# Performance work log

Hardware: AMD Instinct MI355X
Metric: run time of the kernel (lower is better)

Reference implementation:

```python
import jax, jax.numpy as jnp
import numpy as np

V, E, H0, H1 = 32000, 512, 1024, 1024
B, S = 32, 128


def setup_inputs() -> dict:
    key = jax.random.key(0)
    ks = jax.random.split(key, 10)
    s = 0.02
    tokens = jax.random.randint(ks[0], (B, S), 0, V)
    emb = jax.random.normal(ks[1], (V, E), dtype=jnp.float32) * s
    W0 = jax.random.normal(ks[2], (E, H0), dtype=jnp.float32) * s
    U0 = jax.random.normal(ks[3], (H0, H0), dtype=jnp.float32) * s
    b0 = jnp.zeros((H0,), dtype=jnp.float32)
    W1 = jax.random.normal(ks[4], (H0, H1), dtype=jnp.float32) * s
    U1 = jax.random.normal(ks[5], (H1, H1), dtype=jnp.float32) * s
    b1 = jnp.zeros((H1,), dtype=jnp.float32)
    Wd = jax.random.normal(ks[6], (H1, V), dtype=jnp.float32) * s
    bd = jnp.zeros((V,), dtype=jnp.float32)
    return {"tokens": tokens, "emb": emb, "W0": W0, "U0": U0, "b0": b0,
            "W1": W1, "U1": U1, "b1": b1, "Wd": Wd, "bd": bd}


def reference(tokens, emb, W0, U0, b0, W1, U1, b1, Wd, bd):
    # Embedding lookup: [B, S, E]
    x = emb[tokens]
    # Stacked SimpleRNN: h_t = tanh(x W + h U + b), layer1 feeds layer2 per step.
    xt = jnp.swapaxes(x, 0, 1)  # [S, B, E] for scan over time

    def step(carry, x_t):
        h0, h1 = carry
        h0 = jnp.tanh(x_t @ W0 + h0 @ U0 + b0)
        h1 = jnp.tanh(h0 @ W1 + h1 @ U1 + b1)
        return (h0, h1), h1

    batch = tokens.shape[0]
    init = (jnp.zeros((batch, W0.shape[1]), dtype=x.dtype),
            jnp.zeros((batch, W1.shape[1]), dtype=x.dtype))
    _, ys = jax.lax.scan(step, init, xt)  # ys: [S, B, H1]
    ys = jnp.swapaxes(ys, 0, 1)  # [B, S, H1]
    # Final dense to vocab logits: [B, S, V]
    return ys @ Wd + bd
```

## Files before the change

### kernel.cpp

```cpp
#include <hip/hip_runtime.h>
#include <hip/hip_bf16.h>
#include <cstdint>

typedef __attribute__((ext_vector_type(8))) short bf16x8;
typedef __attribute__((ext_vector_type(4))) float f32x4;
typedef __attribute__((ext_vector_type(4))) unsigned int u32x4;

#define V_ 32000
#define E_ 512
#define H_ 1024
#define B_ 32
#define S_ 128

#define L1WG 16
#define L2WG 32
#define NWGS 48

typedef __attribute__((address_space(1))) unsigned int* gas1_t;
typedef __attribute__((address_space(3))) unsigned int* las3_t;
__device__ __forceinline__ void load_lds16(const void* g, void* l) {
  __builtin_amdgcn_global_load_lds((gas1_t)g, (las3_t)l, 16, 0, 0);
}

__device__ __forceinline__ void ldx4_sc(u32x4* d, const void* p) {
  asm volatile("global_load_dwordx4 %0, %1, off sc0 sc1" : "=v"(*d) : "v"(p) : "memory");
}
__device__ __forceinline__ unsigned ld_sc(const unsigned* p) {
  unsigned d;
  asm volatile("global_load_dword %0, %1, off sc0 sc1\n\ts_waitcnt vmcnt(0)"
               : "=v"(d) : "v"(p) : "memory");
  return d;
}
__device__ __forceinline__ void st_swap(unsigned* p, unsigned v) {
  asm volatile("global_atomic_swap %0, %1, off sc1" :: "v"(p), "v"(v) : "memory");
}
__device__ __forceinline__ void st_swap2(uint2* p, uint2 v) {
  asm volatile("global_atomic_swap_x2 %0, %1, off sc1" :: "v"(p), "v"(v) : "memory");
}
#define WAITVM0()                                     \
  asm volatile("s_waitcnt vmcnt(0)" ::: "memory");    \
  __builtin_amdgcn_sched_barrier(0)

__device__ __forceinline__ unsigned short bfbits(float x) {
  __hip_bfloat16 b = __float2bfloat16(x);
  union { __hip_bfloat16 b; unsigned short u; } c;
  c.b = b;
  return c.u;
}

__device__ __forceinline__ uint2 pack_rows(const float f[4], int lane, int j) {
  uint2 v2[4];
#pragma unroll
  for (int r = 0; r < 4; ++r) {
    const float o = __shfl_xor(f[r], 1);
    const float lo = (lane & 1) ? o : f[r];
    const float hi = (lane & 1) ? f[r] : o;
    const unsigned pk = (unsigned)bfbits(lo) | ((unsigned)bfbits(hi) << 16);
    const unsigned q2 = __shfl_xor(pk, 2);
    v2[r].x = (j & 2) ? q2 : pk;
    v2[r].y = (j & 2) ? pk : q2;
  }
  const int rs = lane & 3;
  return rs == 0 ? v2[0] : rs == 1 ? v2[1] : rs == 2 ? v2[2] : v2[3];
}

__global__ __launch_bounds__(256) void transpose_f32_bf16(
    const float* __restrict__ src, __hip_bfloat16* __restrict__ dst, int R, int C) {
  __shared__ float tile[32][33];
  const int c0 = blockIdx.x << 5, r0 = blockIdx.y << 5;
  const int tx = threadIdx.x & 31, ty = threadIdx.x >> 5;
#pragma unroll
  for (int i = 0; i < 32; i += 8)
    tile[ty + i][tx] = src[(size_t)(r0 + ty + i) * C + (c0 + tx)];
  __syncthreads();
#pragma unroll
  for (int i = 0; i < 32; i += 8)
    dst[(size_t)(c0 + ty + i) * R + (r0 + tx)] = __float2bfloat16(tile[tx][ty + i]);
}

__global__ __launch_bounds__(256) void gather_embed(
    const int* __restrict__ tokens, const float* __restrict__ emb,
    __hip_bfloat16* __restrict__ Xg) {
  const int r = blockIdx.x;
  const int t = r >> 5, b = r & 31;
  const int tok = tokens[b * S_ + t];
  const float* e = emb + (size_t)tok * E_;
  __hip_bfloat16* o = Xg + (size_t)r * E_;
  for (int k = threadIdx.x; k < E_; k += 256) o[k] = __float2bfloat16(e[k]);
}

__global__ __launch_bounds__(256) void make_frag_w(
    const float* __restrict__ W, __hip_bfloat16* __restrict__ F) {
  const int idx = blockIdx.x * 256 + threadIdx.x;
  const int lane = idx & 63, kb = (idx >> 6) & 31, g = idx >> 11;
  const int j = (g << 4) + (lane & 15);
  const int kbase = (kb << 5) + ((lane >> 4) << 3);
  __hip_bfloat16* o = F + (size_t)idx * 8;
#pragma unroll
  for (int e = 0; e < 8; ++e) o[e] = __float2bfloat16(W[(size_t)(kbase + e) * H_ + j]);
}

__global__ __launch_bounds__(256) void gemm_bf16_tn(
    const __hip_bfloat16* __restrict__ A, const __hip_bfloat16* __restrict__ Bt,
    const float* __restrict__ bias, float* __restrict__ C, int M, int N, int K) {
  __shared__ __hip_bfloat16 ldsA[128 * 64];
  __shared__ __hip_bfloat16 ldsB[128 * 64];
  const int nwg = gridDim.x * gridDim.y;
  int L = blockIdx.y * gridDim.x + blockIdx.x;
  L = ((L & 7) * (nwg >> 3)) + (L >> 3);
  const int m0 = (L / gridDim.x) << 7;
  const int n0 = (L % gridDim.x) << 7;
  const int tid = threadIdx.x, wave = tid >> 6, lane = tid & 63;
  const int wr = wave >> 1, wc = wave & 1;
  f32x4 acc[4][4];
#pragma unroll
  for (int i = 0; i < 4; ++i)
#pragma unroll
    for (int jj = 0; jj < 4; ++jj) acc[i][jj] = (f32x4){0.f, 0.f, 0.f, 0.f};

  for (int k0 = 0; k0 < K; k0 += 64) {
#pragma unroll
    for (int i = 0; i < 4; ++i) {
      const int c = i * 4 + wave;
      const int idx = (c << 6) + lane;
      const int row = idx >> 3, kk = (idx & 7) << 3;
      load_lds16(A + (size_t)(m0 + row) * K + (k0 + kk), ldsA + c * 512);
      load_lds16(Bt + (size_t)(n0 + row) * K + (k0 + kk), ldsB + c * 512);
    }
    __syncthreads();
#pragma unroll
    for (int ks = 0; ks < 2; ++ks) {
      bf16x8 af[4], bfr[4];
#pragma unroll
      for (int mi = 0; mi < 4; ++mi)
        af[mi] = *(const bf16x8*)(ldsA + (((wr << 6) + (mi << 4) + (lane & 15)) << 6) +
                                  (ks << 5) + ((lane >> 4) << 3));
#pragma unroll
      for (int ni = 0; ni < 4; ++ni)
        bfr[ni] = *(const bf16x8*)(ldsB + (((wc << 6) + (ni << 4) + (lane & 15)) << 6) +
                                   (ks << 5) + ((lane >> 4) << 3));
#pragma unroll
      for (int mi = 0; mi < 4; ++mi)
#pragma unroll
        for (int ni = 0; ni < 4; ++ni)
          acc[mi][ni] =
              __builtin_amdgcn_mfma_f32_16x16x32_bf16(af[mi], bfr[ni], acc[mi][ni], 0, 0, 0);
    }
    __syncthreads();
  }
#pragma unroll
  for (int mi = 0; mi < 4; ++mi) {
#pragma unroll
    for (int ni = 0; ni < 4; ++ni) {
      const int n = n0 + (wc << 6) + (ni << 4) + (lane & 15);
      const float bn = bias[n];
#pragma unroll
      for (int r = 0; r < 4; ++r) {
        const int m = m0 + (wr << 6) + (mi << 4) + ((lane >> 4) << 2) + r;
        C[(size_t)m * N + n] = acc[mi][ni][r] + bn;
      }
    }
  }
}

__global__ __launch_bounds__(512, 2) void rnn_recur(
    const __hip_bfloat16* __restrict__ U0f, const __hip_bfloat16* __restrict__ W1f,
    const __hip_bfloat16* __restrict__ U1f, const float* __restrict__ xw,
    const float* __restrict__ b1,
    __hip_bfloat16* __restrict__ h0buf,
    __hip_bfloat16* __restrict__ h1buf,
    __hip_bfloat16* __restrict__ Y,
    unsigned* __restrict__ flags) {
  __shared__ char smem[135168];
  char* sA0 = smem;
  char* sA1 = smem + 65536;
  float* pad = (float*)(smem + 131072);

  const int g = blockIdx.x;
  const bool isL1 = (g < L1WG);
  const int tid = threadIdx.x, wave = tid >> 6, lane = tid & 63;
  const int mi = wave & 1;
  const int cg = isL1 ? (wave >> 1) : ((wave >> 1) & 1);
  const int mat = isL1 ? 0 : (wave >> 2);
  const int colbase = isL1 ? (g << 6) : ((g - L1WG) << 5);
  const int j = colbase + (cg << 4) + (lane & 15);
  const int gg = (colbase >> 4) + cg;
  const int rowbase = (mi << 4) + ((lane >> 4) << 2);
  const int rs = lane & 3;
  const int ra = (mi << 4) + (lane & 15);
  const int q4 = (lane >> 4) << 4;
  const float b1j = b1[j];

  const __hip_bfloat16* wb = isL1 ? U0f : (mat == 0 ? W1f : U1f);
  bf16x8 wfr[32];
#pragma unroll
  for (int kb = 0; kb < 32; ++kb)
    wfr[kb] = *(const bf16x8*)(wb + (size_t)((((gg << 5) + kb) << 6) + lane) * 8);

  if (!isL1) {
    for (int i = tid; i < 4096; i += 512) *(uint4*)(sA1 + i * 16) = (uint4){0u, 0u, 0u, 0u};
  }
  __syncthreads();

  const int stg_row = tid >> 7;
  const int stg_colb = (tid & 127) << 4;
  const unsigned* fpoll = flags + ((lane < NWGS ? lane : NWGS - 1) << 4);

  if (isL1) {
    for (int p = 0; p < S_; ++p) {
      const float* xrow = xw + ((size_t)p << 15);
      float xv[4];
#pragma unroll
      for (int r = 0; r < 4; ++r) xv[r] = xrow[(rowbase + r) * H_ + j];
      if (p >= 1) {
        const unsigned tgt =
            (lane < L1WG) ? (unsigned)p : (p >= 3 ? (unsigned)(p - 3) : 0u);
        unsigned v;
        do { v = ld_sc(fpoll); } while (__any(v < tgt));
        const char* src0 = (const char*)(h0buf + ((size_t)((p - 1) & 3) << 15));
        u32x4 t0[8];
#pragma unroll
        for (int i = 0; i < 8; ++i) ldx4_sc(&t0[i], src0 + (size_t)(((i << 9) + tid) << 4));
        WAITVM0();
#pragma unroll
        for (int i = 0; i < 8; ++i) {
          const int row = stg_row + (i << 2);
          *(u32x4*)(sA0 + (row << 11) + (stg_colb ^ ((row & 7) << 4))) = t0[i];
        }
        __syncthreads();
      }
      f32x4 acc = {0.f, 0.f, 0.f, 0.f};
      if (p >= 1) {
#pragma unroll
        for (int kb = 0; kb < 32; ++kb) {
          bf16x8 a = *(const bf16x8*)(
              sA0 + (ra << 11) + ((((kb << 6) + q4)) ^ ((ra & 7) << 4)));
          acc = __builtin_amdgcn_mfma_f32_16x16x32_bf16(a, wfr[kb], acc, 0, 0, 0);
        }
      }
      float f[4];
#pragma unroll
      for (int r = 0; r < 4; ++r) f[r] = tanhf(acc[r] + xv[r]);
      uint2 vsel = pack_rows(f, lane, j);
      uint2* h4 = (uint2*)(h0buf + ((size_t)(p & 3) << 15));
      st_swap2(h4 + (rowbase + rs) * (H_ / 4) + (j >> 2), vsel);
      WAITVM0();
      __syncthreads();
      if (tid == 0) st_swap(flags + (g << 4), (unsigned)(p + 1));
    }
  } else {
    for (int t = 0; t < S_; ++t) {
      {
        const unsigned tgt = (lane < L1WG) ? (unsigned)(t + 1) : (unsigned)t;
        unsigned v;
        do { v = ld_sc(fpoll); } while (__any(v < tgt));
      }
      {
        const char* src0 = (const char*)(h0buf + ((size_t)(t & 3) << 15));
        u32x4 t0[8], t1[8];
#pragma unroll
        for (int i = 0; i < 8; ++i) ldx4_sc(&t0[i], src0 + (size_t)(((i << 9) + tid) << 4));
        if (t >= 1) {
          const char* src1 = (const char*)(h1buf + ((size_t)((t - 1) & 1) << 15));
#pragma unroll
          for (int i = 0; i < 8; ++i) ldx4_sc(&t1[i], src1 + (size_t)(((i << 9) + tid) << 4));
        }
        WAITVM0();
#pragma unroll
        for (int i = 0; i < 8; ++i) {
          const int row = stg_row + (i << 2);
          *(u32x4*)(sA0 + (row << 11) + (stg_colb ^ ((row & 7) << 4))) = t0[i];
        }
        if (t >= 1) {
#pragma unroll
          for (int i = 0; i < 8; ++i) {
            const int row = stg_row + (i << 2);
            *(u32x4*)(sA1 + (row << 11) + (stg_colb ^ ((row & 7) << 4))) = t1[i];
          }
        }
        __syncthreads();
      }
      const char* sA = (mat == 0) ? sA0 : sA1;
      f32x4 acc = {0.f, 0.f, 0.f, 0.f};
#pragma unroll
      for (int kb = 0; kb < 32; ++kb) {
        bf16x8 a = *(const bf16x8*)(
            sA + (ra << 11) + ((((kb << 6) + q4)) ^ ((ra & 7) << 4)));
        acc = __builtin_amdgcn_mfma_f32_16x16x32_bf16(a, wfr[kb], acc, 0, 0, 0);
      }
      const int pair = wave & 3;
      if (mat == 0) *(f32x4*)(pad + pair * 256 + lane * 4) = acc;
      __syncthreads();
      if (mat == 1) {
        f32x4 accW = *(const f32x4*)(pad + pair * 256 + lane * 4);
        float f[4];
#pragma unroll
        for (int r = 0; r < 4; ++r) f[r] = tanhf(acc[r] + accW[r] + b1j);
        uint2 vsel = pack_rows(f, lane, j);
        const int bb = rowbase + rs;
        ((uint2*)Y)[((size_t)bb * S_ + t) * (H_ / 4) + (j >> 2)] = vsel;
        uint2* h4 = (uint2*)(h1buf + ((size_t)(t & 1) << 15));
        st_swap2(h4 + bb * (H_ / 4) + (j >> 2), vsel);
      }
      WAITVM0();
      __syncthreads();
      if (tid == 0) st_swap(flags + (g << 4), (unsigned)(t + 1));
    }
  }
}

extern "C" void kernel_launch(void* const* d_in, const int* in_sizes, int n_in, void* d_out,
                              int out_size, void* d_ws, size_t ws_size, hipStream_t stream) {
  const int* tokens = (const int*)d_in[0];
  const float* emb = (const float*)d_in[1];
  const float* W0 = (const float*)d_in[2];
  const float* U0 = (const float*)d_in[3];
  const float* b0 = (const float*)d_in[4];
  const float* W1 = (const float*)d_in[5];
  const float* U1 = (const float*)d_in[6];
  const float* b1 = (const float*)d_in[7];
  const float* Wd = (const float*)d_in[8];
  const float* bd = (const float*)d_in[9];
  float* out = (float*)d_out;

  char* ws = (char*)d_ws;
  __hip_bfloat16* Wdt = (__hip_bfloat16*)ws;  ws += (size_t)V_ * H_ * 2;
  __hip_bfloat16* W0t = (__hip_bfloat16*)ws;  ws += (size_t)H_ * E_ * 2;
  __hip_bfloat16* Xg = (__hip_bfloat16*)ws;   ws += (size_t)4096 * E_ * 2;
  __hip_bfloat16* U0f = (__hip_bfloat16*)ws;  ws += (size_t)H_ * H_ * 2;
  __hip_bfloat16* W1f = (__hip_bfloat16*)ws;  ws += (size_t)H_ * H_ * 2;
  __hip_bfloat16* U1f = (__hip_bfloat16*)ws;  ws += (size_t)H_ * H_ * 2;
  float* xw = (float*)ws;                     ws += (size_t)4096 * H_ * 4;
  __hip_bfloat16* h0buf = (__hip_bfloat16*)ws; ws += 4 * B_ * H_ * 2;
  __hip_bfloat16* h1buf = (__hip_bfloat16*)ws; ws += 2 * B_ * H_ * 2;
  __hip_bfloat16* Y = (__hip_bfloat16*)ws;    ws += (size_t)4096 * H_ * 2;
  unsigned* flags = (unsigned*)ws;            ws += 4096;

  transpose_f32_bf16<<<dim3(V_ / 32, H_ / 32), 256, 0, stream>>>(Wd, Wdt, H_, V_);
  transpose_f32_bf16<<<dim3(H_ / 32, E_ / 32), 256, 0, stream>>>(W0, W0t, E_, H_);
  gather_embed<<<4096, 256, 0, stream>>>(tokens, emb, Xg);
  make_frag_w<<<512, 256, 0, stream>>>(U0, U0f);
  make_frag_w<<<512, 256, 0, stream>>>(W1, W1f);
  make_frag_w<<<512, 256, 0, stream>>>(U1, U1f);
  hipMemsetAsync(flags, 0, 4096, stream);

  gemm_bf16_tn<<<dim3(H_ / 128, 4096 / 128), 256, 0, stream>>>(Xg, W0t, b0, xw, 4096, H_, E_);

  rnn_recur<<<NWGS, 512, 0, stream>>>(U0f, W1f, U1f, xw, b1, h0buf, h1buf, Y, flags);

  gemm_bf16_tn<<<dim3(V_ / 128, 4096 / 128), 256, 0, stream>>>(Y, Wdt, bd, out, 4096, V_, H_);
}
```

Before: 1.263 ms.

## Overlap layer-1 recurrent matmul with wait for layer-0 state; remap vocab GEMM tiles

Layer-1 workgroups now wait only for the previous step's h1, load it, and compute the h1·U1 product before polling for the current step's h0 from layer 0. This takes the recurrent half of the layer-1 work off the critical path behind layer 0, at the cost of an extra barrier and a second flag poll per step. Separately, the vocab-projection GEMM (N=32000) now walks M tiles fastest in place of the swizzled order, so consecutive workgroups share the same Wd columns for better cache reuse.

Result: slower. 1.364 ms (+8.0%).

```diff
diff --git a/kernel.cpp b/kernel.cpp
--- a/kernel.cpp
+++ b/kernel.cpp
@@ -107,9 +107,16 @@
   __shared__ __hip_bfloat16 ldsB[128 * 64];
   const int nwg = gridDim.x * gridDim.y;
   int L = blockIdx.y * gridDim.x + blockIdx.x;
-  L = ((L & 7) * (nwg >> 3)) + (L >> 3);
-  const int m0 = (L / gridDim.x) << 7;
-  const int n0 = (L % gridDim.x) << 7;
+  int m0, n0;
+  if (N == 32000) {
+    const int mtiles = M >> 7;
+    m0 = (L % mtiles) << 7;
+    n0 = (L / mtiles) << 7;
+  } else {
+    L = ((L & 7) * (nwg >> 3)) + (L >> 3);
+    m0 = (L / gridDim.x) << 7;
+    n0 = (L % gridDim.x) << 7;
+  }
   const int tid = threadIdx.x, wave = tid >> 6, lane = tid & 63;
   const int wr = wave >> 1, wc = wave & 1;
   f32x4 acc[4][4];
@@ -250,52 +257,66 @@
     }
   } else {
     for (int t = 0; t < S_; ++t) {
-      {
-        const unsigned tgt = (lane < L1WG) ? (unsigned)(t + 1) : (unsigned)t;
+      if (t >= 1) {
+        const unsigned tgt = (lane >= L1WG && lane < NWGS) ? (unsigned)t : 0u;
         unsigned v;
         do { v = ld_sc(fpoll); } while (__any(v < tgt));
+        const char* src1 = (const char*)(h1buf + ((size_t)((t - 1) & 1) << 15));
+        u32x4 t1[8];
+#pragma unroll
+        for (int i = 0; i < 8; ++i) ldx4_sc(&t1[i], src1 + (size_t)(((i << 9) + tid) << 4));
+        WAITVM0();
+#pragma unroll
+        for (int i = 0; i < 8; ++i) {
+          const int row = stg_row + (i << 2);
+          *(u32x4*)(sA1 + (row << 11) + (stg_colb ^ ((row & 7) << 4))) = t1[i];
+        }
+        __syncthreads();
+      }
+      f32x4 accU = {0.f, 0.f, 0.f, 0.f};
+      if (mat == 1) {
+#pragma unroll
+        for (int kb = 0; kb < 32; ++kb) {
+          bf16x8 a = *(const bf16x8*)(
+              sA1 + (ra << 11) + ((((kb << 6) + q4)) ^ ((ra & 7) << 4)));
+          accU = __builtin_amdgcn_mfma_f32_16x16x32_bf16(a, wfr[kb], accU, 0, 0, 0);
+        }
+      }
+      {
+        const unsigned tgt = (lane < L1WG) ? (unsigned)(t + 1) : 0u;
+        unsigned v;
+        do { v = ld_sc(fpoll); } while (__any(v < tgt));
       }
       {
         const char* src0 = (const char*)(h0buf + ((size_t)(t & 3) << 15));
-        u32x4 t0[8], t1[8];
+        u32x4 t0[8];
 #pragma unroll
         for (int i = 0; i < 8; ++i) ldx4_sc(&t0[i], src0 + (size_t)(((i << 9) + tid) << 4));
-        if (t >= 1) {
-          const char* src1 = (const char*)(h1buf + ((size_t)((t - 1) & 1) << 15));
-#pragma unroll
-          for (int i = 0; i < 8; ++i) ldx4_sc(&t1[i], src1 + (size_t)(((i << 9) + tid) << 4));
-        }
         WAITVM0();
 #pragma unroll
         for (int i = 0; i < 8; ++i) {
           const int row = stg_row + (i << 2);
           *(u32x4*)(sA0 + (row << 11) + (stg_colb ^ ((row & 7) << 4))) = t0[i];
         }
-        if (t >= 1) {
-#pragma unroll
-          for (int i = 0; i < 8; ++i) {
-            const int row = stg_row + (i << 2);
-            *(u32x4*)(sA1 + (row << 11) + (stg_colb ^ ((row & 7) << 4))) = t1[i];
-          }
-        }
         __syncthreads();
       }
-      const char* sA = (mat == 0) ? sA0 : sA1;
-      f32x4 acc = {0.f, 0.f, 0.f, 0.f};
-#pragma unroll
-      for (int kb = 0; kb < 32; ++kb) {
-        bf16x8 a = *(const bf16x8*)(
-            sA + (ra << 11) + ((((kb << 6) + q4)) ^ ((ra & 7) << 4)));
-        acc = __builtin_amdgcn_mfma_f32_16x16x32_bf16(a, wfr[kb], acc, 0, 0, 0);
-      }
       const int pair = wave & 3;
-      if (mat == 0) *(f32x4*)(pad + pair * 256 + lane * 4) = acc;
+      if (mat == 0) {
+        f32x4 acc = {0.f, 0.f, 0.f, 0.f};
+#pragma unroll
+        for (int kb = 0; kb < 32; ++kb) {
+          bf16x8 a = *(const bf16x8*)(
+              sA0 + (ra << 11) + ((((kb << 6) + q4)) ^ ((ra & 7) << 4)));
+          acc = __builtin_amdgcn_mfma_f32_16x16x32_bf16(a, wfr[kb], acc, 0, 0, 0);
+        }
+        *(f32x4*)(pad + pair * 256 + lane * 4) = acc;
+      }
       __syncthreads();
       if (mat == 1) {
         f32x4 accW = *(const f32x4*)(pad + pair * 256 + lane * 4);
         float f[4];
 #pragma unroll
-        for (int r = 0; r < 4; ++r) f[r] = tanhf(acc[r] + accW[r] + b1j);
+        for (int r = 0; r < 4; ++r) f[r] = tanhf(accU[r] + accW[r] + b1j);
         uint2 vsel = pack_rows(f, lane, j);
         const int bb = rowbase + rs;
         ((uint2*)Y)[((size_t)bb * S_ + t) * (H_ / 4) + (j >> 2)] = vsel;
```

## Halve recurrence workgroups by giving each wave both 16-row batch tiles

Applied to the files above, without the earlier changes.

The persistent RNN recurrence kernel now uses 24 workgroups (8 for layer 0, 16 for layer 1) instead of 48. Each wave computes two 16-row MFMA tiles, covering all 32 batch rows, so it keeps one weight-column fragment set and issues two accumulator chains. The aim is to cut the number of participants in the per-step flag polling and barrier so the cross-workgroup synchronisation on the serial critical path gets cheaper. In exchange, each step does twice the MFMA and LDS work per wave and uses fewer CUs, the padding buffer grows, and occupancy drops to one block per CU.

Measured after the change: 1.570 ms. 24.3% more time.

```diff
diff --git a/kernel.cpp b/kernel.cpp
--- a/kernel.cpp
+++ b/kernel.cpp
@@ -12,9 +12,9 @@
 #define B_ 32
 #define S_ 128
 
-#define L1WG 16
-#define L2WG 32
-#define NWGS 48
+#define NL1 8
+#define NL2 16
+#define NWGS 24
 
 typedef __attribute__((address_space(1))) unsigned int* gas1_t;
 typedef __attribute__((address_space(3))) unsigned int* las3_t;
@@ -163,7 +163,7 @@
   }
 }
 
-__global__ __launch_bounds__(512, 2) void rnn_recur(
+__global__ __launch_bounds__(512, 1) void rnn_recur(
     const __hip_bfloat16* __restrict__ U0f, const __hip_bfloat16* __restrict__ W1f,
     const __hip_bfloat16* __restrict__ U1f, const float* __restrict__ xw,
     const float* __restrict__ b1,
@@ -171,24 +171,30 @@
     __hip_bfloat16* __restrict__ h1buf,
     __hip_bfloat16* __restrict__ Y,
     unsigned* __restrict__ flags) {
-  __shared__ char smem[135168];
+  __shared__ char smem[139264];
   char* sA0 = smem;
   char* sA1 = smem + 65536;
   float* pad = (float*)(smem + 131072);
 
   const int g = blockIdx.x;
-  const bool isL1 = (g < L1WG);
+  const bool isL1 = (g < NL1);
   const int tid = threadIdx.x, wave = tid >> 6, lane = tid & 63;
-  const int mi = wave & 1;
-  const int cg = isL1 ? (wave >> 1) : ((wave >> 1) & 1);
-  const int mat = isL1 ? 0 : (wave >> 2);
-  const int colbase = isL1 ? (g << 6) : ((g - L1WG) << 5);
-  const int j = colbase + (cg << 4) + (lane & 15);
-  const int gg = (colbase >> 4) + cg;
-  const int rowbase = (mi << 4) + ((lane >> 4) << 2);
+
+  int j, gg, mat;
+  if (isL1) {
+    j = (g << 7) + (wave << 4) + (lane & 15);
+    gg = (g << 3) + wave;
+    mat = 0;
+  } else {
+    const int gl = g - NL1;
+    const int cgl = wave & 3;
+    mat = wave >> 2;
+    j = (gl << 6) + (cgl << 4) + (lane & 15);
+    gg = (gl << 2) + cgl;
+  }
+  const int q4 = (lane >> 4) << 4;
   const int rs = lane & 3;
-  const int ra = (mi << 4) + (lane & 15);
-  const int q4 = (lane >> 4) << 4;
+  const int ra0 = lane & 15, ra1 = 16 + (lane & 15);
   const float b1j = b1[j];
 
   const __hip_bfloat16* wb = isL1 ? U0f : (mat == 0 ? W1f : U1f);
@@ -209,12 +215,15 @@
   if (isL1) {
     for (int p = 0; p < S_; ++p) {
       const float* xrow = xw + ((size_t)p << 15);
-      float xv[4];
-#pragma unroll
-      for (int r = 0; r < 4; ++r) xv[r] = xrow[(rowbase + r) * H_ + j];
+      float xv[2][4];
+#pragma unroll
+      for (int mi = 0; mi < 2; ++mi)
+#pragma unroll
+        for (int r = 0; r < 4; ++r)
+          xv[mi][r] = xrow[((mi << 4) + ((lane >> 4) << 2) + r) * H_ + j];
       if (p >= 1) {
         const unsigned tgt =
-            (lane < L1WG) ? (unsigned)p : (p >= 3 ? (unsigned)(p - 3) : 0u);
+            (lane < NL1) ? (unsigned)p : (p >= 3 ? (unsigned)(p - 3) : 0u);
         unsigned v;
         do { v = ld_sc(fpoll); } while (__any(v < tgt));
         const char* src0 = (const char*)(h0buf + ((size_t)((p - 1) & 3) << 15));
@@ -229,21 +238,29 @@
         }
         __syncthreads();
       }
-      f32x4 acc = {0.f, 0.f, 0.f, 0.f};
+      f32x4 a0 = {0.f, 0.f, 0.f, 0.f}, a1 = {0.f, 0.f, 0.f, 0.f};
       if (p >= 1) {
 #pragma unroll
         for (int kb = 0; kb < 32; ++kb) {
-          bf16x8 a = *(const bf16x8*)(
-              sA0 + (ra << 11) + ((((kb << 6) + q4)) ^ ((ra & 7) << 4)));
-          acc = __builtin_amdgcn_mfma_f32_16x16x32_bf16(a, wfr[kb], acc, 0, 0, 0);
-        }
-      }
-      float f[4];
-#pragma unroll
-      for (int r = 0; r < 4; ++r) f[r] = tanhf(acc[r] + xv[r]);
-      uint2 vsel = pack_rows(f, lane, j);
+          bf16x8 f0 = *(const bf16x8*)(sA0 + (ra0 << 11) +
+                                       (((kb << 6) + q4) ^ ((ra0 & 7) << 4)));
+          bf16x8 f1 = *(const bf16x8*)(sA0 + (ra1 << 11) +
+                                       (((kb << 6) + q4) ^ ((ra1 & 7) << 4)));
+          a0 = __builtin_amdgcn_mfma_f32_16x16x32_bf16(f0, wfr[kb], a0, 0, 0, 0);
+          a1 = __builtin_amdgcn_mfma_f32_16x16x32_bf16(f1, wfr[kb], a1, 0, 0, 0);
+        }
+      }
       uint2* h4 = (uint2*)(h0buf + ((size_t)(p & 3) << 15));
-      st_swap2(h4 + (rowbase + rs) * (H_ / 4) + (j >> 2), vsel);
+#pragma unroll
+      for (int mi = 0; mi < 2; ++mi) {
+        f32x4 acc = (mi == 0) ? a0 : a1;
+        float f[4];
+#pragma unroll
+        for (int r = 0; r < 4; ++r) f[r] = tanhf(acc[r] + xv[mi][r]);
+        uint2 vsel = pack_rows(f, lane, j);
+        const int bb = (mi << 4) + ((lane >> 4) << 2) + rs;
+        st_swap2(h4 + bb * (H_ / 4) + (j >> 2), vsel);
+      }
       WAITVM0();
       __syncthreads();
       if (tid == 0) st_swap(flags + (g << 4), (unsigned)(p + 1));
@@ -251,7 +268,7 @@
   } else {
     for (int t = 0; t < S_; ++t) {
       {
-        const unsigned tgt = (lane < L1WG) ? (unsigned)(t + 1) : (unsigned)t;
+        const unsigned tgt = (lane < NL1) ? (unsigned)(t + 1) : (unsigned)t;
         unsigned v;
         do { v = ld_sc(fpoll); } while (__any(v < tgt));
       }
@@ -281,26 +298,37 @@
         __syncthreads();
       }
       const char* sA = (mat == 0) ? sA0 : sA1;
-      f32x4 acc = {0.f, 0.f, 0.f, 0.f};
+      f32x4 a0 = {0.f, 0.f, 0.f, 0.f}, a1 = {0.f, 0.f, 0.f, 0.f};
 #pragma unroll
       for (int kb = 0; kb < 32; ++kb) {
-        bf16x8 a = *(const bf16x8*)(
-            sA + (ra << 11) + ((((kb << 6) + q4)) ^ ((ra & 7) << 4)));
-        acc = __builtin_amdgcn_mfma_f32_16x16x32_bf16(a, wfr[kb], acc, 0, 0, 0);
-      }
-      const int pair = wave & 3;
-      if (mat == 0) *(f32x4*)(pad + pair * 256 + lane * 4) = acc;
+        bf16x8 f0 = *(const bf16x8*)(sA + (ra0 << 11) +
+                                     (((kb << 6) + q4) ^ ((ra0 & 7) << 4)));
+        bf16x8 f1 = *(const bf16x8*)(sA + (ra1 << 11) +
+                                     (((kb << 6) + q4) ^ ((ra1 & 7) << 4)));
+        a0 = __builtin_amdgcn_mfma_f32_16x16x32_bf16(f0, wfr[kb], a0, 0, 0, 0);
+        a1 = __builtin_amdgcn_mfma_f32_16x16x32_bf16(f1, wfr[kb], a1, 0, 0, 0);
+      }
+      const int cgl = wave & 3;
+      if (mat == 0) {
+        *(f32x4*)(pad + (((cgl << 1) + 0) * 64 + lane) * 4) = a0;
+        *(f32x4*)(pad + (((cgl << 1) + 1) * 64 + lane) * 4) = a1;
+      }
       __syncthreads();
       if (mat == 1) {
-        f32x4 accW = *(const f32x4*)(pad + pair * 256 + lane * 4);
-        float f[4];
-#pragma unroll
-        for (int r = 0; r < 4; ++r) f[r] = tanhf(acc[r] + accW[r] + b1j);
-        uint2 vsel = pack_rows(f, lane, j);
-        const int bb = rowbase + rs;
-        ((uint2*)Y)[((size_t)bb * S_ + t) * (H_ / 4) + (j >> 2)] = vsel;
         uint2* h4 = (uint2*)(h1buf + ((size_t)(t & 1) << 15));
-        st_swap2(h4 + bb * (H_ / 4) + (j >> 2), vsel);
+        uint2* Y4 = (uint2*)Y;
+#pragma unroll
+        for (int mi = 0; mi < 2; ++mi) {
+          f32x4 accW = *(const f32x4*)(pad + (((cgl << 1) + mi) * 64 + lane) * 4);
+          f32x4 accU = (mi == 0) ? a0 : a1;
+          float f[4];
+#pragma unroll
+          for (int r = 0; r < 4; ++r) f[r] = tanhf(accU[r] + accW[r] + b1j);
+          uint2 vsel = pack_rows(f, lane, j);
+          const int bb = (mi << 4) + ((lane >> 4) << 2) + rs;
+          st_swap2(h4 + bb * (H_ / 4) + (j >> 2), vsel);
+          Y4[((size_t)bb * S_ + t) * (H_ / 4) + (j >> 2)] = vsel;
+        }
       }
       WAITVM0();
       __syncthreads();
```
